# Kernel optimization log

Measured on AMD Instinct MI355X. Metric: run time of the kernel, lower is better.

Reference implementation:

```python
import jax, jax.numpy as jnp
import numpy as np

B, T, F, K = 32, 1500, 512, 31
QBITS = 8
EPS = 1e-5


def fake_quant(x, bits=QBITS):
    """Symmetric per-tensor fake quantization (scale from dynamic max-abs),
    with straight-through estimator so gradients pass through unchanged."""
    qmax = 2.0 ** (bits - 1) - 1.0  # 127 for 8 bits
    scale = jnp.maximum(jnp.max(jnp.abs(x)) / qmax, 1e-8)
    q = jnp.clip(jnp.round(x / scale), -qmax - 1.0, qmax) * scale
    return x + jax.lax.stop_gradient(q - x)


def setup_inputs() -> dict:
    key = jax.random.key(0)
    ks = jax.random.split(key, 5)
    x = jax.random.normal(ks[0], (B, T, F), dtype=jnp.float32)
    W1 = jax.random.normal(ks[1], (2 * F, F), dtype=jnp.float32) * (1.0 / np.sqrt(F))
    b1 = jnp.zeros((2 * F,), jnp.float32)
    dw_w = jax.random.normal(ks[2], (F, 1, K), dtype=jnp.float32) * (1.0 / np.sqrt(K))
    dw_b = jnp.zeros((F,), jnp.float32)
    W2 = jax.random.normal(ks[3], (F, F), dtype=jnp.float32) * (1.0 / np.sqrt(F))
    b2 = jnp.zeros((F,), jnp.float32)
    return {
        "x": x,
        "ln_gamma": jnp.ones((F,), jnp.float32),
        "ln_beta": jnp.zeros((F,), jnp.float32),
        "W1": W1, "b1": b1,
        "dw_w": dw_w, "dw_b": dw_b,
        "bn_gamma": jnp.ones((F,), jnp.float32),
        "bn_beta": jnp.zeros((F,), jnp.float32),
        "W2": W2, "b2": b2,
    }


def _forward(x, ln_gamma, ln_beta, W1, b1, dw_w, dw_b, bn_gamma, bn_beta, W2, b2):
    # LayerNorm over last dim F
    mu = jnp.mean(x, axis=-1, keepdims=True)
    var = jnp.mean(jnp.square(x - mu), axis=-1, keepdims=True)
    t = (x - mu) * jax.lax.rsqrt(var + EPS) * ln_gamma + ln_beta

    # pconv1 in-quant -> quantized pointwise conv1 (Linear F -> 2F) -> out-quant
    t = fake_quant(t)
    t = jnp.einsum("btf,gf->btg", t, fake_quant(W1)) + b1
    t = fake_quant(t)

    # GLU over last dim: [B,T,2F] -> [B,T,F]
    a, g = jnp.split(t, 2, axis=-1)
    t = a * jax.nn.sigmoid(g)

    # depthwise conv on [B,F,T]
    t = jnp.transpose(t, (0, 2, 1))  # [B,F,T]
    t = fake_quant(t)
    t = jax.lax.conv_general_dilated(
        t, fake_quant(dw_w),
        window_strides=(1,),
        padding=[((K - 1) // 2, (K - 1) // 2)],
        feature_group_count=F,
        dimension_numbers=("NCH", "OIH", "NCH"),
    ) + dw_b[None, :, None]
    t = fake_quant(t)

    # BatchNorm1d over channel dim (stats over batch and time), training-style batch stats
    bmu = jnp.mean(t, axis=(0, 2), keepdims=True)
    bvar = jnp.mean(jnp.square(t - bmu), axis=(0, 2), keepdims=True)
    t = (t - bmu) * jax.lax.rsqrt(bvar + EPS) * bn_gamma[None, :, None] + bn_beta[None, :, None]

    t = jnp.transpose(t, (0, 2, 1))  # [B,T,F]
    t = jax.nn.silu(t)

    # pconv2 in-quant -> quantized pointwise conv2 (Linear F -> F) -> out-quant
    t = fake_quant(t)
    t = jnp.einsum("btf,gf->btg", t, fake_quant(W2)) + b2
    t = fake_quant(t)
    return t  # dropout is identity (p=0 / eval)


def reference(x, ln_gamma, ln_beta, W1, b1, dw_w, dw_b, bn_gamma, bn_beta, W2, b2):
    return _forward(x, ln_gamma, ln_beta, W1, b1, dw_w, dw_b, bn_gamma, bn_beta, W2, b2)
```

## Files before the change

kernel.cpp:

```cpp
#include <hip/hip_runtime.h>
#include <stdint.h>

typedef __bf16 bf16;
typedef float    fx4    __attribute__((ext_vector_type(4)));
typedef int      ix2    __attribute__((ext_vector_type(2)));
typedef int      ix4    __attribute__((ext_vector_type(4)));

#define NB 32
#define NT 1500
#define NF 512
#define NM (NB*NT)
#define KW 31
#define EPSF 1e-5f

__device__ __forceinline__ float dscale(const float* a) {
  return fmaxf(a[0] * (1.0f/127.0f), 1e-8f);
}
__device__ __forceinline__ float fq_int(float x, float inv_s) {
  return fminf(fmaxf(rintf(x*inv_s), -128.0f), 127.0f);
}
__device__ __forceinline__ void block_amax(float v, float* dst) {
  __shared__ float red[8];
  #pragma unroll
  for (int o = 32; o > 0; o >>= 1) v = fmaxf(v, __shfl_xor(v, o));
  if ((threadIdx.x & 63) == 0) red[threadIdx.x >> 6] = v;
  __syncthreads();
  if (threadIdx.x == 0) {
    int nw = blockDim.x >> 6;
    float m = red[0];
    for (int i = 1; i < nw; i++) m = fmaxf(m, red[i]);
    atomicMax((unsigned int*)dst, __float_as_uint(m));
  }
}

__device__ __forceinline__ float amax_loop(const float* p, long n4, int bid, int gsz) {
  float am = 0.f;
  long i = (long)bid * blockDim.x + threadIdx.x;
  long stride = (long)gsz * blockDim.x;
  for (; i < n4; i += stride) {
    fx4 v = ((const fx4*)p)[i];
    #pragma unroll
    for (int j = 0; j < 4; j++) am = fmaxf(am, fabsf(v[j]));
  }
  return am;
}
__global__ void absmax_w(const float* __restrict__ W1, const float* __restrict__ W2,
                         const float* __restrict__ dwp, float* a) {
  int bx = blockIdx.x;
  float am; float* dst;
  if (bx < 256)      { am = amax_loop(W1,  131072, bx,       256); dst = a + 1; }
  else if (bx < 384) { am = amax_loop(W2,  65536,  bx - 256, 128); dst = a + 2; }
  else               { am = amax_loop(dwp, 3968,   bx - 384, 8);   dst = a + 3; }
  block_amax(am, dst);
}

__global__ void quant_pack_i8(const float* __restrict__ src, char* __restrict__ dst,
                              int R, const float* amax) {
  float inv_s = 1.0f / dscale(amax);
  int total = R * 32;
  for (int t = blockIdx.x*blockDim.x + threadIdx.x; t < total; t += gridDim.x*blockDim.x) {
    int r = t >> 5, q16 = t & 31;
    const float* s = src + (size_t)r*512 + q16*16;
    ix4 o;
    #pragma unroll
    for (int g = 0; g < 4; g++) {
      fx4 v = *(const fx4*)(s + g*4);
      int wrd = 0;
      #pragma unroll
      for (int j = 0; j < 4; j++) wrd |= ((int)fq_int(v[j], inv_s) & 0xff) << (8*j);
      o[g] = wrd;
    }
    int r16 = r >> 4, m16 = r & 15, kb = q16 >> 2, quad = q16 & 3;
    size_t chunk = ((size_t)r16*8 + kb)*64 + quad*16 + m16;
    ((ix4*)dst)[chunk] = o;
  }
}

__global__ void quant_deq_f32(float* __restrict__ p, long n4, const float* amax) {
  float s = dscale(amax);
  float inv_s = 1.0f / s;
  long i = (long)blockIdx.x * blockDim.x + threadIdx.x;
  long stride = (long)gridDim.x * blockDim.x;
  for (; i < n4; i += stride) {
    fx4 v = ((fx4*)p)[i];
    fx4 o;
    #pragma unroll
    for (int j = 0; j < 4; j++) o[j] = fq_int(v[j], inv_s) * s;
    ((fx4*)p)[i] = o;
  }
}

__global__ void ln_amax_k(const float* __restrict__ x, const float* __restrict__ g,
                          const float* __restrict__ be, float* amax) {
  int lane = threadIdx.x & 63;
  int wavesTotal = (gridDim.x * blockDim.x) >> 6;
  int wave = ((blockIdx.x * blockDim.x) + threadIdx.x) >> 6;
  fx4 g0 = ((const fx4*)g)[2*lane],  g1 = ((const fx4*)g)[2*lane+1];
  fx4 b0 = ((const fx4*)be)[2*lane], b1v = ((const fx4*)be)[2*lane+1];
  float gf[8], bff[8];
  #pragma unroll
  for (int j = 0; j < 4; j++) { gf[j] = g0[j]; gf[4+j] = g1[j]; bff[j] = b0[j]; bff[4+j] = b1v[j]; }
  float am = 0.f;
  for (int row = wave; row < NM; row += wavesTotal) {
    const fx4* xr = (const fx4*)(x + (long)row*NF);
    fx4 x0 = xr[2*lane], x1 = xr[2*lane+1];
    float xf[8]; float s = 0.f;
    #pragma unroll
    for (int j = 0; j < 4; j++) { xf[j] = x0[j]; xf[4+j] = x1[j]; }
    #pragma unroll
    for (int j = 0; j < 8; j++) s += xf[j];
    #pragma unroll
    for (int o = 32; o > 0; o >>= 1) s += __shfl_xor(s, o);
    float mu = s * (1.0f/NF);
    float vs = 0.f;
    #pragma unroll
    for (int j = 0; j < 8; j++) { float d = xf[j]-mu; vs += d*d; }
    #pragma unroll
    for (int o = 32; o > 0; o >>= 1) vs += __shfl_xor(vs, o);
    float inv = rsqrtf(vs*(1.0f/NF) + EPSF);
    #pragma unroll
    for (int j = 0; j < 8; j++) {
      float v = (xf[j]-mu)*inv*gf[j] + bff[j];
      am = fmaxf(am, fabsf(v));
    }
  }
  block_amax(am, amax);
}

__global__ void ln_pack_k(const float* __restrict__ x, const float* __restrict__ g,
                          const float* __restrict__ be, char* __restrict__ dst,
                          const float* amax) {
  int lane = threadIdx.x & 63;
  int wavesTotal = (gridDim.x * blockDim.x) >> 6;
  int wave = ((blockIdx.x * blockDim.x) + threadIdx.x) >> 6;
  float inv_s = 1.0f / dscale(amax);
  fx4 g0 = ((const fx4*)g)[2*lane],  g1 = ((const fx4*)g)[2*lane+1];
  fx4 b0 = ((const fx4*)be)[2*lane], b1v = ((const fx4*)be)[2*lane+1];
  float gf[8], bff[8];
  #pragma unroll
  for (int j = 0; j < 4; j++) { gf[j] = g0[j]; gf[4+j] = g1[j]; bff[j] = b0[j]; bff[4+j] = b1v[j]; }
  for (int row = wave; row < NM; row += wavesTotal) {
    const fx4* xr = (const fx4*)(x + (long)row*NF);
    fx4 x0 = xr[2*lane], x1 = xr[2*lane+1];
    float xf[8]; float s = 0.f;
    #pragma unroll
    for (int j = 0; j < 4; j++) { xf[j] = x0[j]; xf[4+j] = x1[j]; }
    #pragma unroll
    for (int j = 0; j < 8; j++) s += xf[j];
    #pragma unroll
    for (int o = 32; o > 0; o >>= 1) s += __shfl_xor(s, o);
    float mu = s * (1.0f/NF);
    float vs = 0.f;
    #pragma unroll
    for (int j = 0; j < 8; j++) { float d = xf[j]-mu; vs += d*d; }
    #pragma unroll
    for (int o = 32; o > 0; o >>= 1) vs += __shfl_xor(vs, o);
    float inv = rsqrtf(vs*(1.0f/NF) + EPSF);
    int lo = 0, hi = 0;
    #pragma unroll
    for (int j = 0; j < 4; j++) {
      float v = (xf[j]-mu)*inv*gf[j] + bff[j];
      lo |= ((int)fq_int(v, inv_s) & 0xff) << (8*j);
    }
    #pragma unroll
    for (int j = 0; j < 4; j++) {
      float v = (xf[4+j]-mu)*inv*gf[4+j] + bff[4+j];
      hi |= ((int)fq_int(v, inv_s) & 0xff) << (8*j);
    }
    size_t chunk = ((size_t)(row>>4)*8 + (lane>>3))*64 + ((lane>>1)&3)*16 + (row&15);
    *(ix2*)(dst + chunk*16 + (lane&1)*8) = ix2{lo, hi};
  }
}

template<int NBN, int MODE>
__global__ __launch_bounds__(256) void gemm_k(
    const char* __restrict__ A, const char* __restrict__ Bt,
    const float* __restrict__ bias, float* __restrict__ C,
    const float* amaxA, const float* amaxB, float* amaxC) {
  const int N = NBN * 128;
  int id = blockIdx.x;
  int bn = (id >> 3) % NBN;
  int bm = 8 * (id / (8 * NBN)) + (id & 7);
  if (bm >= 375) return;
  int lane = threadIdx.x & 63;
  int w = threadIdx.x >> 6;
  int wm = w >> 1, wn = w & 1;
  int quad = lane >> 4;
  int m16 = lane & 15;

  __shared__ __align__(16) float ebuf[2][32][132];

  ix4 acc[4][4];
  #pragma unroll
  for (int i = 0; i < 4; i++)
    #pragma unroll
    for (int j = 0; j < 4; j++) acc[i][j] = ix4{0,0,0,0};

  const char* pA[4];
  const char* pB[4];
  #pragma unroll
  for (int i = 0; i < 4; i++)
    pA[i] = A + (size_t)(bm*8 + wm*4 + i)*8192 + lane*16;
  #pragma unroll
  for (int j = 0; j < 4; j++)
    pB[j] = Bt + (size_t)(bn*8 + wn*4 + j)*8192 + lane*16;

  #pragma unroll
  for (int kb = 0; kb < 8; kb++) {
    ix4 aF[4], bF[4];
    #pragma unroll
    for (int i = 0; i < 4; i++) aF[i] = *(const ix4*)(pA[i] + kb*1024);
    #pragma unroll
    for (int j = 0; j < 4; j++) bF[j] = *(const ix4*)(pB[j] + kb*1024);
    #pragma unroll
    for (int i = 0; i < 4; i++)
      #pragma unroll
      for (int j = 0; j < 4; j++) {
        if (MODE == 0)
          acc[i][j] = __builtin_amdgcn_mfma_i32_16x16x64_i8(aF[i], bF[j], acc[i][j], 0, 0, 0);
        else
          acc[i][j] = __builtin_amdgcn_mfma_i32_16x16x64_i8(bF[j], aF[i], acc[i][j], 0, 0, 0);
      }
  }

  float ab = dscale(amaxA) * dscale(amaxB);
  float am = 0.f;
  const int h     = (MODE == 0) ? wn : wm;
  const int other = (MODE == 0) ? wm : wn;

  #pragma unroll
  for (int rnd = 0; rnd < 2; rnd++) {
    __syncthreads();
    if (MODE == 0) {
      #pragma unroll
      for (int jj = 0; jj < 2; jj++) {
        int j = rnd*2 + jj;
        int col = bn*128 + wn*64 + j*16 + m16;
        float bv = bias[col];
        #pragma unroll
        for (int i = 0; i < 4; i++) {
          fx4 o;
          #pragma unroll
          for (int rr = 0; rr < 4; rr++) {
            float v = (float)acc[i][j][rr]*ab + bv;
            am = fmaxf(am, fabsf(v)); o[rr] = v;
          }
          *(fx4*)&ebuf[h][jj*16 + m16][wm*64 + i*16 + quad*4] = o;
        }
      }
    } else {
      #pragma unroll
      for (int ii = 0; ii < 2; ii++) {
        int i = rnd*2 + ii;
        #pragma unroll
        for (int j = 0; j < 4; j++) {
          int n0 = bn*128 + wn*64 + j*16 + quad*4;
          fx4 bv = *(const fx4*)(bias + n0);
          fx4 o;
          #pragma unroll
          for (int rr = 0; rr < 4; rr++) {
            float v = (float)acc[i][j][rr]*ab + bv[rr];
            am = fmaxf(am, fabsf(v)); o[rr] = v;
          }
          *(fx4*)&ebuf[h][ii*16 + m16][wn*64 + j*16 + quad*4] = o;
        }
      }
    }
    __syncthreads();
    #pragma unroll
    for (int it = 0; it < 8; it++) {
      int lrow = other*16 + it*2 + (lane >> 5);
      int cf = (lane & 31) * 4;
      fx4 o = *(const fx4*)&ebuf[h][lrow][cf];
      int orow = ((MODE == 0) ? bn*128 : bm*128) + h*64 + rnd*32 + lrow;
      size_t base = (MODE == 0) ? ((size_t)orow*NM + (size_t)bm*128 + cf)
                                : ((size_t)orow*N  + (size_t)bn*128 + cf);
      *(fx4*)(C + base) = o;
    }
  }
  block_amax(am, amaxC);
}

__global__ void glu_k(const float* __restrict__ uT, float* __restrict__ v,
                      const float* amaxU, float* amaxV) {
  float s = dscale(amaxU);
  float inv_s = 1.0f / s;
  float am = 0.f;
  const int tid = threadIdx.x;
  const int npairs = (NB*NF)/2;
  for (int pr = blockIdx.x; pr < npairs; pr += gridDim.x) {
    int row0 = pr*2;
    for (int i = tid; i < 750; i += 256) {
      int r2 = (i >= 375) ? 1 : 0;
      int c = i - 375*r2;
      int row = row0 + r2;
      int b = row >> 9, f = row & (NF-1);
      long bt = (long)b*NT + c*4;
      fx4 a = *(const fx4*)(uT + (long)f*NM + bt);
      fx4 g = *(const fx4*)(uT + (long)(f+NF)*NM + bt);
      fx4 o;
      #pragma unroll
      for (int j = 0; j < 4; j++) {
        float av = fq_int(a[j], inv_s) * s;
        float gv = fq_int(g[j], inv_s) * s;
        float val = av * (1.0f/(1.0f + expf(-gv)));
        am = fmaxf(am, fabsf(val));
        o[j] = val;
      }
      *(fx4*)(v + (long)row*NT + c*4) = o;
    }
  }
  block_amax(am, amaxV);
}

__global__ void dwconv_k(const float* __restrict__ v, const float* __restrict__ w,
                         const float* __restrict__ wb, float* __restrict__ y,
                         const float* amaxV, const float* amaxW, float* amaxY) {
  __shared__ float z[2][1568];
  __shared__ float wl[2][32];
  float sv = dscale(amaxV); float inv_sv = 1.0f/sv;
  float sw = dscale(amaxW); float inv_sw = 1.0f/sw;
  float am = 0.f;
  const int tid = threadIdx.x;
  const int rr = tid >> 7;
  const int cl = tid & 127;
  const int npairs = (NB*NF)/2;
  for (int pr = blockIdx.x; pr < npairs; pr += gridDim.x) {
    int row0 = pr*2;
    __syncthreads();
    if (tid < 64) {
      int r2 = tid >> 5, k = tid & 31;
      if (k < KW) {
        int f = (row0 + r2) & (NF-1);
        wl[r2][k] = fq_int(w[f*KW + k], inv_sw) * sw;
      }
    }
    if (tid < 128) {
      int r2 = tid >> 6, jj = tid & 63;
      if (jj < 16) z[r2][jj] = 0.f;
      else         z[r2][1500 + jj] = 0.f;
    }
    const fx4* vp = (const fx4*)(v + (long)row0 * NT);
    for (int i = tid; i < 750; i += 256) {
      fx4 q = vp[i];
      int r2 = (i >= 375) ? 1 : 0;
      int ii = i - 375*r2;
      fx4 o;
      #pragma unroll
      for (int j = 0; j < 4; j++) o[j] = fq_int(q[j], inv_sv) * sv;
      *(fx4*)&z[r2][16 + 4*ii] = o;
    }
    __syncthreads();
    float wr[KW];
    #pragma unroll
    for (int k = 0; k < KW; k++) wr[k] = wl[rr][k];
    float bias = wb[(row0 + rr) & (NF-1)];
    long base = (long)(row0 + rr) * NT;
    #pragma unroll
    for (int pass = 0; pass < 3; pass++) {
      int c = cl + pass*128;
      if (c < 375) {
        int t0 = c*4;
        fx4 win[9];
        #pragma unroll
        for (int i = 0; i < 9; i++) win[i] = *(const fx4*)&z[rr][t0 + 4*i];
        float acc0 = bias, acc1 = bias, acc2 = bias, acc3 = bias;
        #pragma unroll
        for (int k = 0; k < KW; k++) {
          float wk = wr[k];
          acc0 += win[(k+1)>>2][(k+1)&3] * wk;
          acc1 += win[(k+2)>>2][(k+2)&3] * wk;
          acc2 += win[(k+3)>>2][(k+3)&3] * wk;
          acc3 += win[(k+4)>>2][(k+4)&3] * wk;
        }
        fx4 o = {acc0, acc1, acc2, acc3};
        #pragma unroll
        for (int j = 0; j < 4; j++) am = fmaxf(am, fabsf(o[j]));
        *(fx4*)&y[base + t0] = o;
      }
    }
  }
  block_amax(am, amaxY);
}

__global__ void bnstats_part_k(const float* __restrict__ y, const float* amaxY,
                               int* s1a, int* s2a, unsigned* qmxa, unsigned* qmna) {
  float sy = dscale(amaxY); float inv_sy = 1.0f/sy;
  int f = blockIdx.x & 511;
  int part = blockIdx.x >> 9;
  int s1 = 0, s2 = 0, qmn = 127, qmx = -128;
  for (int b = part*8; b < part*8 + 8; b++) {
    const fx4* base = (const fx4*)(y + ((long)b*NF + f)*NT);
    for (int i = threadIdx.x; i < NT/4; i += blockDim.x) {
      fx4 v = base[i];
      #pragma unroll
      for (int j = 0; j < 4; j++) {
        int q = (int)fq_int(v[j], inv_sy);
        s1 += q; s2 += q*q;
        qmn = min(qmn, q); qmx = max(qmx, q);
      }
    }
  }
  #pragma unroll
  for (int o = 32; o > 0; o >>= 1) {
    s1 += __shfl_xor(s1, o); s2 += __shfl_xor(s2, o);
    qmn = min(qmn, __shfl_xor(qmn, o)); qmx = max(qmx, __shfl_xor(qmx, o));
  }
  __shared__ int rs1[4], rs2[4], rmn[4], rmx[4];
  if ((threadIdx.x & 63) == 0) {
    int wv = threadIdx.x >> 6;
    rs1[wv] = s1; rs2[wv] = s2; rmn[wv] = qmn; rmx[wv] = qmx;
  }
  __syncthreads();
  if (threadIdx.x == 0) {
    int S1 = rs1[0]+rs1[1]+rs1[2]+rs1[3];
    int S2 = rs2[0]+rs2[1]+rs2[2]+rs2[3];
    int mn = min(min(rmn[0],rmn[1]), min(rmn[2],rmn[3]));
    int mx = max(max(rmx[0],rmx[1]), max(rmx[2],rmx[3]));
    atomicAdd(s1a + f, S1);
    atomicAdd(s2a + f, S2);
    atomicMax(qmxa + f, (unsigned)(mx + 128));
    atomicMax(qmna + f, (unsigned)(127 - mn));
  }
}

__global__ void bnfin_k(const int* __restrict__ s1a, const int* __restrict__ s2a,
                        const unsigned* __restrict__ qmxa, const unsigned* __restrict__ qmna,
                        const float* amaxY, const float* __restrict__ bg,
                        const float* __restrict__ bb,
                        float* bn_mean, float* bn_rinv, float* amaxP) {
  int f = blockIdx.x;
  float sy = dscale(amaxY);
  __shared__ float sh_mean, sh_rinv; __shared__ int sh_qmn, sh_qmx;
  if (threadIdx.x == 0) {
    long long S1 = s1a[f];
    long long S2 = s2a[f];
    double s = (double)sy;
    double mean = (double)S1 * s / (double)NM;
    double var  = (double)S2 * s * s / (double)NM - mean*mean;
    float fm = (float)mean;
    float fr = rsqrtf((float)var + EPSF);
    bn_mean[f] = fm; bn_rinv[f] = fr;
    sh_mean = fm; sh_rinv = fr;
    sh_qmx = (int)qmxa[f] - 128;
    sh_qmn = 127 - (int)qmna[f];
  }
  __syncthreads();
  float pm = 0.f;
  int q = sh_qmn + (int)threadIdx.x;
  if (q <= sh_qmx) {
    float zq = (float)q * sy;
    float val = (zq - sh_mean)*sh_rinv*bg[f] + bb[f];
    val = val / (1.0f + expf(-val));
    pm = fabsf(val);
  }
  block_amax(pm, amaxP);
}

__global__ void bnsilu_pack_k(const float* __restrict__ y, const float* __restrict__ bg,
                              const float* __restrict__ bb, const float* amaxY,
                              const float* bn_mean, const float* bn_rinv,
                              char* __restrict__ pq, const float* amaxP) {
  __shared__ float lds[32][33];
  float sy = dscale(amaxY); float inv_sy = 1.0f/sy;
  float inv_sp = 1.0f / dscale(amaxP);
  int tx = threadIdx.x & 31, ty = threadIdx.x >> 5;
  const int TTILES = (NT + 31)/32;
  const int ntile = NB * (NF/32) * TTILES;
  for (int tile = blockIdx.x; tile < ntile; tile += gridDim.x) {
    int b = tile / ((NF/32)*TTILES);
    int rem = tile % ((NF/32)*TTILES);
    int fT = rem / TTILES, tT = rem % TTILES;
    int f0 = fT*32, t0 = tT*32;
    __syncthreads();
    #pragma unroll
    for (int sI = 0; sI < 4; sI++) {
      int f = f0 + ty + sI*8;
      int t = t0 + tx;
      if (t < NT) {
        float zq = fq_int(y[((long)b*NF + f)*NT + t], inv_sy) * sy;
        float val = (zq - bn_mean[f])*bn_rinv[f]*bg[f] + bb[f];
        val = val / (1.0f + expf(-val));
        lds[tx][ty + sI*8] = val;
      }
    }
    __syncthreads();
    if (threadIdx.x < 128) {
      int r = threadIdx.x >> 2;
      int c = threadIdx.x & 3;
      int t = t0 + r;
      if (t < NT) {
        int lo = 0, hi = 0;
        #pragma unroll
        for (int j = 0; j < 4; j++)
          lo |= ((int)fq_int(lds[r][c*8 + j],     inv_sp) & 0xff) << (8*j);
        #pragma unroll
        for (int j = 0; j < 4; j++)
          hi |= ((int)fq_int(lds[r][c*8 + 4 + j], inv_sp) & 0xff) << (8*j);
        long bt = (long)b*NT + t;
        int q8 = (f0 >> 3) + c;
        size_t chunk = ((size_t)(bt>>4)*8 + (q8>>3))*64 + ((q8>>1)&3)*16 + (bt&15);
        *(ix2*)(pq + chunk*16 + (q8&1)*8) = ix2{lo, hi};
      }
    }
  }
}

extern "C" void kernel_launch(void* const* d_in, const int* in_sizes, int n_in,
                              void* d_out, int out_size, void* d_ws, size_t ws_size,
                              hipStream_t stream) {
  const float* x  = (const float*)d_in[0];
  const float* lg = (const float*)d_in[1];
  const float* lb = (const float*)d_in[2];
  const float* W1 = (const float*)d_in[3];
  const float* b1 = (const float*)d_in[4];
  const float* dw = (const float*)d_in[5];
  const float* db = (const float*)d_in[6];
  const float* bg = (const float*)d_in[7];
  const float* bb = (const float*)d_in[8];
  const float* W2 = (const float*)d_in[9];
  const float* b2 = (const float*)d_in[10];
  float* out = (float*)d_out;

  char* ws = (char*)d_ws;
  float* amax    = (float*)ws;
  float* bn_mean = (float*)(ws + 1024);
  float* bn_rinv = (float*)(ws + 4096);
  int*      s1a  = (int*)(ws + 8192);
  int*      s2a  = (int*)(ws + 10240);
  unsigned* qmxa = (unsigned*)(ws + 12288);
  unsigned* qmna = (unsigned*)(ws + 14336);
  char* H = ws + 16384;
  float* uT    = (float*)H;
  char*  t_q   = H + 196608000;
  float* y     = (float*)H;
  char*  p_q   = H + 221184000;
  char*  W1q   = H + 245760000;
  char*  W2q   = H + 246284288;
  float* v = (float*)d_out;
  float* r = (float*)d_out;

  hipMemsetAsync(ws, 0, 16384, stream);

  absmax_w<<<392, 256, 0, stream>>>(W1, W2, dw, amax);
  quant_pack_i8<<<128, 256, 0, stream>>>(W1, W1q, 1024, amax+1);
  quant_pack_i8<<<64,  256, 0, stream>>>(W2, W2q, 512,  amax+2);

  ln_amax_k<<<1536, 256, 0, stream>>>(x, lg, lb, amax+0);
  ln_pack_k<<<3072, 256, 0, stream>>>(x, lg, lb, t_q, amax+0);
  gemm_k<8,0><<<3008, 256, 0, stream>>>(t_q, W1q, b1, uT, amax+0, amax+1, amax+4);
  glu_k<<<4096, 256, 0, stream>>>(uT, v, amax+4, amax+5);
  dwconv_k<<<8192, 256, 0, stream>>>(v, dw, db, y, amax+5, amax+3, amax+6);
  bnstats_part_k<<<2048, 256, 0, stream>>>(y, amax+6, s1a, s2a, qmxa, qmna);
  bnfin_k<<<512, 256, 0, stream>>>(s1a, s2a, qmxa, qmna, amax+6, bg, bb, bn_mean, bn_rinv, amax+7);
  bnsilu_pack_k<<<4096, 256, 0, stream>>>(y, bg, bb, amax+6, bn_mean, bn_rinv, p_q, amax+7);
  gemm_k<4,1><<<1504, 256, 0, stream>>>(p_q, W2q, b2, r, amax+7, amax+2, amax+8);
  quant_deq_f32<<<2048, 256, 0, stream>>>(out, 24576000/4, amax+8);
}
```

Before: 591.4 us.

## Software-pipeline dwconv row loads with register prefetch across a fixed grid

The depthwise conv kernel now runs on a fixed grid of 2048 blocks, each handling four row pairs. While it computes the current pair out of LDS, it prefetches the next pair's input and weights from global memory into registers. This hides global load latency behind the convolution math and cuts the number of block launches. The cost is higher register pressure and an extra barrier per iteration, and the hardcoded grid size and iteration count are tied to exactly 8192 row pairs.

```diff
diff --git a/kernel.cpp b/kernel.cpp
--- a/kernel.cpp
+++ b/kernel.cpp
@@ -324,38 +324,60 @@
   const int tid = threadIdx.x;
   const int rr = tid >> 7;
   const int cl = tid & 127;
-  const int npairs = (NB*NF)/2;
-  for (int pr = blockIdx.x; pr < npairs; pr += gridDim.x) {
-    int row0 = pr*2;
-    __syncthreads();
-    if (tid < 64) {
-      int r2 = tid >> 5, k = tid & 31;
-      if (k < KW) {
-        int f = (row0 + r2) & (NF-1);
-        wl[r2][k] = fq_int(w[f*KW + k], inv_sw) * sw;
-      }
-    }
-    if (tid < 128) {
-      int r2 = tid >> 6, jj = tid & 63;
-      if (jj < 16) z[r2][jj] = 0.f;
-      else         z[r2][1500 + jj] = 0.f;
-    }
-    const fx4* vp = (const fx4*)(v + (long)row0 * NT);
-    for (int i = tid; i < 750; i += 256) {
-      fx4 q = vp[i];
-      int r2 = (i >= 375) ? 1 : 0;
-      int ii = i - 375*r2;
-      fx4 o;
-      #pragma unroll
-      for (int j = 0; j < 4; j++) o[j] = fq_int(q[j], inv_sv) * sv;
-      *(fx4*)&z[r2][16 + 4*ii] = o;
-    }
-    __syncthreads();
+  const int wr2 = tid >> 5, wkk = tid & 31;
+
+  if (tid < 128) {
+    int r2 = tid >> 6, jj = tid & 63;
+    if (jj < 16) z[r2][jj] = 0.f;
+    else         z[r2][1500 + jj] = 0.f;
+  }
+
+  fx4 st[3];
+  float wreg = 0.f;
+
+  {
+    long vb = (long)(blockIdx.x*2) * NT;
+    #pragma unroll
+    for (int k = 0; k < 3; k++) {
+      int i = tid + k*256;
+      if (i < 750) st[k] = *(const fx4*)(v + vb + i*4);
+    }
+    if (tid < 64 && wkk < KW)
+      wreg = w[((blockIdx.x*2 + wr2) & (NF-1))*KW + wkk];
+    #pragma unroll
+    for (int k = 0; k < 3; k++) {
+      int i = tid + k*256;
+      if (i < 750) {
+        int r2 = (i >= 375) ? 1 : 0;
+        int ii = i - 375*r2;
+        fx4 o;
+        #pragma unroll
+        for (int j = 0; j < 4; j++) o[j] = fq_int(st[k][j], inv_sv) * sv;
+        *(fx4*)&z[r2][16 + 4*ii] = o;
+      }
+    }
+    if (tid < 64 && wkk < KW) wl[wr2][wkk] = fq_int(wreg, inv_sw) * sw;
+  }
+  __syncthreads();
+
+  #pragma unroll
+  for (int idx = 0; idx < 4; idx++) {
+    int p = blockIdx.x + idx*2048;
+    if (idx < 3) {
+      long vb = (long)((p + 2048)*2) * NT;
+      #pragma unroll
+      for (int k = 0; k < 3; k++) {
+        int i = tid + k*256;
+        if (i < 750) st[k] = *(const fx4*)(v + vb + i*4);
+      }
+      if (tid < 64 && wkk < KW)
+        wreg = w[(((p + 2048)*2 + wr2) & (NF-1))*KW + wkk];
+    }
     float wr[KW];
     #pragma unroll
     for (int k = 0; k < KW; k++) wr[k] = wl[rr][k];
-    float bias = wb[(row0 + rr) & (NF-1)];
-    long base = (long)(row0 + rr) * NT;
+    float bias = wb[(p*2 + rr) & (NF-1)];
+    long base = (long)(p*2 + rr) * NT;
     #pragma unroll
     for (int pass = 0; pass < 3; pass++) {
       int c = cl + pass*128;
@@ -378,6 +400,23 @@
         for (int j = 0; j < 4; j++) am = fmaxf(am, fabsf(o[j]));
         *(fx4*)&y[base + t0] = o;
       }
+    }
+    __syncthreads();
+    if (idx < 3) {
+      #pragma unroll
+      for (int k = 0; k < 3; k++) {
+        int i = tid + k*256;
+        if (i < 750) {
+          int r2 = (i >= 375) ? 1 : 0;
+          int ii = i - 375*r2;
+          fx4 o;
+          #pragma unroll
+          for (int j = 0; j < 4; j++) o[j] = fq_int(st[k][j], inv_sv) * sv;
+          *(fx4*)&z[r2][16 + 4*ii] = o;
+        }
+      }
+      if (tid < 64 && wkk < KW) wl[wr2][wkk] = fq_int(wreg, inv_sw) * sw;
+      __syncthreads();
     }
   }
   block_amax(am, amaxY);
@@ -550,7 +589,7 @@
   ln_pack_k<<<3072, 256, 0, stream>>>(x, lg, lb, t_q, amax+0);
   gemm_k<8,0><<<3008, 256, 0, stream>>>(t_q, W1q, b1, uT, amax+0, amax+1, amax+4);
   glu_k<<<4096, 256, 0, stream>>>(uT, v, amax+4, amax+5);
-  dwconv_k<<<8192, 256, 0, stream>>>(v, dw, db, y, amax+5, amax+3, amax+6);
+  dwconv_k<<<2048, 256, 0, stream>>>(v, dw, db, y, amax+5, amax+3, amax+6);
   bnstats_part_k<<<2048, 256, 0, stream>>>(y, amax+6, s1a, s2a, qmxa, qmna);
   bnfin_k<<<512, 256, 0, stream>>>(s1a, s2a, qmxa, qmna, amax+6, bg, bb, bn_mean, bn_rinv, amax+7);
   bnsilu_pack_k<<<4096, 256, 0, stream>>>(y, bg, bb, amax+6, bn_mean, bn_rinv, p_q, amax+7);
```

New measurement: 548.7 us. 1.08x faster.
